# Performance work log

Measured on AMD Instinct MI355X. Metric: run time of the kernel, lower is better.

The kernel has to match this reference:

```python
import jax, jax.numpy as jnp
import numpy as np

SIDE = 64; EMB = 16; CH = 64; K = 64; V = 64; L = 8
N = SIDE * SIDE

def _pos_table(side, d):
    pe = np.array([[p / np.power(10000, 2 * (j // 2) / d) for j in range(d)]
                   if p != 0 else np.zeros(d) for p in range(side)])
    pe[1:, 0::2] = np.sin(pe[1:, 0::2])
    pe[1:, 1::2] = np.cos(pe[1:, 1::2])
    return pe.astype(np.float32)  # [side, d]

def _pos_emb():
    # Replicates torch .view(1, emb, side, 1): plain reshape of [side, emb] -> [emb, side]
    t = _pos_table(SIDE, EMB).reshape(EMB, SIDE)
    xe = np.broadcast_to(t[:, :, None], (EMB, SIDE, SIDE))
    ye = np.broadcast_to(t[:, None, :], (EMB, SIDE, SIDE))
    return jnp.asarray(np.concatenate([xe, ye], 0).reshape(1, 2 * EMB, N))

def _conv_mask():
    # CausalConv mask, see_center=False, 5x5: zero center pixel onward in center row, and all rows below
    m = np.ones((CH, 3, 5, 5), np.float32)
    m[:, :, 2, 2:] = 0.0
    m[:, :, 3:, :] = 0.0
    return jnp.asarray(m)

def _lrelu(x):
    return jnp.where(x >= 0, x, 0.01 * x)  # LeakyReLU(0.01)

def _bn(x, g, b, eps=1e-5):
    # training-mode batch norm (biased variance), channel axis = 1
    axes = (0,) + tuple(range(2, x.ndim))
    m = jnp.mean(x, axes, keepdims=True)
    var = jnp.mean((x - m) ** 2, axes, keepdims=True)
    sh = (1, -1) + (1,) * (x.ndim - 2)
    return g.reshape(sh) * (x - m) / jnp.sqrt(var + eps) + b.reshape(sh)

def _cv1(w, b, x):
    # 1x1 Conv1d: [O,I] x [B,I,N] -> [B,O,N]
    return jnp.einsum('oi,bin->bon', w, x) + b[:, None]

def reference(x, conv_w, conv_b, bn0_g, bn0_b, q_w, q_b, fk_w, fk_b, ck_w, ck_b,
              fv_w, fv_b, cv_w, cv_b, bn_g, bn_b, out_w, out_b):
    B = x.shape[0]
    pos = jnp.broadcast_to(_pos_emb(), (B, 2 * EMB, N))
    mask = jnp.tril(jnp.ones((N, N), jnp.float32))

    # masked causal conv input layer + BN + LeakyReLU
    w = conv_w * _conv_mask()
    h = jax.lax.conv_general_dilated(x, w, (1, 1), [(2, 2), (2, 2)],
                                     dimension_numbers=('NCHW', 'OIHW', 'NCHW'))
    h = h + conv_b[None, :, None, None]
    h = _lrelu(_bn(h, bn0_g, bn0_b)).reshape(B, CH, N)

    k0 = jnp.zeros((B, K, N), x.dtype)
    v0 = jnp.zeros((B, V, N), x.dtype)
    inv_sqrt_k = 1.0 / jnp.sqrt(jnp.float32(K))

    def layer(carry, p):
        h, k, v = carry
        qw, qb, fkw, fkb, ckw, ckb, fvw, fvb, cvw, cvb, g, bb = p
        x0 = jnp.concatenate([h, pos], 1)            # [B, CH+32, N]
        x0k = jnp.concatenate([x0, k], 1)            # [B, 160, N]
        x0v = jnp.concatenate([x0, v], 1)
        fk = jax.nn.sigmoid(_cv1(fkw, fkb, x0k))
        ck = _lrelu(_cv1(ckw, ckb, x0k))
        k_new = fk * k + ck                          # highway-gated persistent K
        fv = jax.nn.sigmoid(_cv1(fvw, fvb, x0v))
        cv_ = _lrelu(_cv1(cvw, cvb, x0v))
        v_new = fv * v + cv_
        q = _lrelu(_cv1(qw, qb, x0))                 # [B, K, N]
        attn = jnp.einsum('bkn,bkm->bnm', q, k) * inv_sqrt_k  # uses OLD k
        attn = attn * mask + (1.0 - mask) * (-10000.0)
        attn = jax.nn.softmax(attn, axis=-1) * mask
        out1 = jnp.einsum('bnm,bvm->bvn', attn, v)   # uses OLD v; [B, V, N]
        # original code computes fc(out1) but discards it (out2 overwritten)
        h2 = _lrelu(_bn(out1, g, bb))
        return (h2, k_new, v_new), None

    params = (q_w, q_b, fk_w, fk_b, ck_w, ck_b, fv_w, fv_b, cv_w, cv_b, bn_g, bn_b)
    (h, k, v), _ = jax.lax.scan(layer, (h, k0, v0), params)

    out = jnp.einsum('oi,bin->bon', out_w, h) + out_b[None, :, None]
    return out.reshape(B, out_w.shape[0], SIDE, SIDE)

def setup_inputs() -> dict:
    key = jax.random.key(0)
    ks = jax.random.split(key, 12)
    s = 0.05
    return {
        'x': jax.random.normal(ks[0], (2, 3, 64, 64), jnp.float32),
        'conv_w': jax.random.normal(ks[1], (CH, 3, 5, 5), jnp.float32) * s,
        'conv_b': jnp.zeros((CH,), jnp.float32),
        'bn0_g': jnp.ones((CH,), jnp.float32),
        'bn0_b': jnp.zeros((CH,), jnp.float32),
        'q_w': jax.random.normal(ks[2], (L, K, CH + 2 * EMB), jnp.float32) * s,
        'q_b': jnp.zeros((L, K), jnp.float32),
        'fk_w': jax.random.normal(ks[3], (L, K, CH + K + 2 * EMB), jnp.float32) * s,
        'fk_b': jnp.zeros((L, K), jnp.float32),
        'ck_w': jax.random.normal(ks[4], (L, K, CH + K + 2 * EMB), jnp.float32) * s,
        'ck_b': jnp.zeros((L, K), jnp.float32),
        'fv_w': jax.random.normal(ks[5], (L, V, CH + V + 2 * EMB), jnp.float32) * s,
        'fv_b': jnp.zeros((L, V), jnp.float32),
        'cv_w': jax.random.normal(ks[6], (L, V, CH + V + 2 * EMB), jnp.float32) * s,
        'cv_b': jnp.zeros((L, V), jnp.float32),
        'bn_g': jnp.ones((L, CH), jnp.float32),
        'bn_b': jnp.zeros((L, CH), jnp.float32),
        'out_w': jax.random.normal(ks[7], (100, V), jnp.float32) * s,
        'out_b': jnp.zeros((100,), jnp.float32),
    }
```

## Files before the change

kernel.cpp:

```cpp
#include <hip/hip_runtime.h>

#define NPIX 4096
#define CHN  64

typedef __attribute__((ext_vector_type(8))) short short8;
typedef __attribute__((ext_vector_type(8))) unsigned short ushort8;
typedef __attribute__((ext_vector_type(4))) unsigned short ushort4v;
typedef __attribute__((ext_vector_type(4))) float f32x4;
typedef __attribute__((ext_vector_type(16))) float f32x16;
typedef __attribute__((ext_vector_type(4))) unsigned int uint4v;

__device__ __forceinline__ float lrelu_(float x){ return x >= 0.f ? x : 0.01f*x; }

__device__ __forceinline__ unsigned short f2bf(float x){
  union { float f; unsigned u; } v; v.f = x;
  unsigned r = v.u + 0x7FFF + ((v.u >> 16) & 1);
  return (unsigned short)(r >> 16);
}
__device__ __forceinline__ float bf2f(unsigned short h){
  union { unsigned u; float f; } v; v.u = ((unsigned)h) << 16;
  return v.f;
}
__device__ __forceinline__ float asf_(unsigned u){
  union { unsigned u; float f; } v; v.u = u; return v.f;
}

__global__ void pos_kernel(float* __restrict__ pos){
  int idx = blockIdx.x*256 + threadIdx.x;
  int c = idx >> 12;
  int n = idx & (NPIX-1);
  int bcoord = (c < 16) ? (n >> 6) : (n & 63);
  int a = (c < 16) ? c : (c - 16);
  int flat = a*64 + bcoord;
  int p = flat >> 4;
  int j = flat & 15;
  float val = 0.f;
  if (p != 0){
    float ex = (float)(j & ~1) * (1.f/16.f);
    float w = powf(10000.f, -ex);
    float ang = (float)p * w;
    val = (j & 1) ? cosf(ang) : sinf(ang);
  }
  pos[idx] = val;
}

__global__ void wtr_kernel(const float* __restrict__ qw, const float* __restrict__ fkw,
                           const float* __restrict__ ckw, const float* __restrict__ fvw,
                           const float* __restrict__ cvw, const float* __restrict__ convw,
                           float* __restrict__ wt){
  int idx = blockIdx.x*256 + threadIdx.x;
  if (idx >= 381632) return;
  if (idx < 49152){
    int l = idx / 6144, r = idx % 6144, i = r >> 6, o = r & 63;
    wt[idx] = qw[(l*64 + o)*96 + i];
  } else if (idx < 376832){
    int e = idx - 49152;
    int mat = e / 81920, r = e % 81920;
    int l = r / 10240, rr = r % 10240, i = rr >> 6, o = rr & 63;
    const float* src = (mat==0) ? fkw : (mat==1) ? ckw : (mat==2) ? fvw : cvw;
    wt[idx] = src[(l*64 + o)*160 + i];
  } else {
    int e = idx - 376832;
    int o = e & 63, tap = e >> 6;
    int ci = tap / 25, r = tap % 25;
    wt[idx] = convw[(o*3 + ci)*25 + r];
  }
}

__global__ __launch_bounds__(256) void conv_in_kernel(const float* __restrict__ x,
                                                      const float* __restrict__ cwt,
                                                      const float* __restrict__ cb,
                                                      float* __restrict__ out){
  int t = threadIdx.x;
  int o = t & 63;
  int sub = t >> 6;
  int bid = blockIdx.x;
  int b = bid >> 10;
  int n = ((bid & 1023) << 2) + sub;
  int y = n >> 6, xx = n & 63;
  float acc = cb[o];
  #pragma unroll
  for (int ci=0; ci<3; ++ci){
    const float* xp = x + ((b*3+ci)<<12);
    #pragma unroll
    for (int ky=0; ky<3; ++ky){
      int yy = y + ky - 2;
      if (yy < 0) continue;
      int nk = (ky==2) ? 2 : 5;
      #pragma unroll
      for (int kx=0; kx<5; ++kx){
        if (kx >= nk) break;
        int xc = xx + kx - 2;
        if (xc < 0 || xc > 63) continue;
        acc += xp[(yy<<6) + xc] * cwt[(ci*25 + ky*5 + kx)*64 + o];
      }
    }
  }
  out[(b*CHN+o)*NPIX + n] = acc;
}

__global__ __launch_bounds__(1024) void bn_stats_kernel(const float* __restrict__ xin,
                                                        float* __restrict__ stats){
  int c = blockIdx.x;
  int t = threadIdx.x;
  float s = 0.f, ss = 0.f;
  #pragma unroll
  for (int it=0; it<8; ++it){
    int idx = t + it*1024;
    float v = xin[(((idx>>12))*CHN + c)*NPIX + (idx & (NPIX-1))];
    s += v; ss += v*v;
  }
  #pragma unroll
  for (int o=1; o<64; o<<=1){ s += __shfl_xor(s,o); ss += __shfl_xor(ss,o); }
  __shared__ float ps[16], pq[16];
  if ((t & 63) == 0){ ps[t>>6] = s; pq[t>>6] = ss; }
  __syncthreads();
  if (t == 0){
    float S=0.f, Q=0.f;
    #pragma unroll
    for (int i=0;i<16;++i){ S += ps[i]; Q += pq[i]; }
    float mu = S*(1.f/8192.f);
    float var = Q*(1.f/8192.f) - mu*mu;
    var = fmaxf(var, 0.f);
    stats[c*2]   = mu;
    stats[c*2+1] = rsqrtf(var + 1e-5f);
  }
}

__global__ void bn_apply_kernel(const float* __restrict__ xin, const float* __restrict__ stats,
                                const float* __restrict__ g, const float* __restrict__ bb,
                                float* __restrict__ hout){
  int idx = blockIdx.x*256 + threadIdx.x;
  int e = idx << 2;
  int c = (e >> 12) & 63;
  float mu = stats[c*2], rstd = stats[c*2+1];
  float gain = g[c]*rstd;
  float beta = bb[c] - gain*mu;
  float4 v = *(const float4*)(xin + e);
  float4 r;
  r.x = lrelu_(gain*v.x + beta);
  r.y = lrelu_(gain*v.y + beta);
  r.z = lrelu_(gain*v.z + beta);
  r.w = lrelu_(gain*v.w + beta);
  *(float4*)(hout + e) = r;
}

__global__ __launch_bounds__(256) void bn_apply2_kernel(float* __restrict__ hbuf,
                                                        const float* __restrict__ psum,
                                                        const float* __restrict__ psq,
                                                        const float* __restrict__ g,
                                                        const float* __restrict__ bb){
  int bid = blockIdx.x;
  int ebase = bid << 10;
  int c = (ebase >> 12) & 63;
  int t = threadIdx.x;
  float s = psum[c*256 + t];
  float q = psq[c*256 + t];
  #pragma unroll
  for (int o=1; o<64; o<<=1){ s += __shfl_xor(s,o); q += __shfl_xor(q,o); }
  __shared__ float as[4], aq[4];
  if ((t & 63) == 0){ as[t>>6] = s; aq[t>>6] = q; }
  __syncthreads();
  float S = as[0]+as[1]+as[2]+as[3];
  float Q = aq[0]+aq[1]+aq[2]+aq[3];
  float mu = S*(1.f/8192.f);
  float var = fmaxf(Q*(1.f/8192.f) - mu*mu, 0.f);
  float rstd = rsqrtf(var + 1e-5f);
  float gain = g[c]*rstd;
  float beta = bb[c] - gain*mu;
  float4 v = *(const float4*)(hbuf + ebase + t*4);
  float4 r;
  r.x = lrelu_(gain*v.x + beta);
  r.y = lrelu_(gain*v.y + beta);
  r.z = lrelu_(gain*v.z + beta);
  r.w = lrelu_(gain*v.w + beta);
  *(float4*)(hbuf + ebase + t*4) = r;
}

__global__ __launch_bounds__(256) void cv1_kernel(
    const float* __restrict__ hbuf, const float* __restrict__ pos,
    const float* __restrict__ kold, const float* __restrict__ vold,
    const float* __restrict__ qwt,
    const float* __restrict__ fkwt, const float* __restrict__ ckwt,
    const float* __restrict__ fvwt, const float* __restrict__ cvwt,
    const float* __restrict__ qbi,  const float* __restrict__ fkb,
    const float* __restrict__ ckb,  const float* __restrict__ fvb,
    const float* __restrict__ cvb,
    unsigned short* __restrict__ qh, unsigned short* __restrict__ ql,
    float* __restrict__ knew, unsigned short* __restrict__ khn, unsigned short* __restrict__ kln,
    float* __restrict__ vnew, unsigned short* __restrict__ vhTn, unsigned short* __restrict__ vlTn)
{
  int t = threadIdx.x;
  int o  = t & 63;
  int wv = t >> 6;
  int b    = blockIdx.x >> 8;
  int tile = blockIdx.x & 255;
  int n0 = tile*16 + wv*4;

  const float* hb = hbuf + b*CHN*NPIX + n0;
  const float* kb = kold + b*CHN*NPIX + n0;
  const float* vb = vold + b*CHN*NPIX + n0;
  const float* pb = pos + n0;

  auto load4 = [&](const float* p, float* dst){
    float4 a = *(const float4*)p;
    dst[0]=a.x; dst[1]=a.y; dst[2]=a.z; dst[3]=a.w;
  };

  float x[4];
  long obase = (long)(b*CHN+o)*NPIX + n0;
  size_t nbase = ((size_t)b*NPIX + n0)*64 + o;

  {
    float aq[4];
    float bias = qbi[o];
    #pragma unroll
    for (int j=0;j<4;++j) aq[j]=bias;
    #pragma unroll 4
    for (int i=0;i<64;++i){
      load4(hb + i*NPIX, x);
      float w = qwt[i*64 + o];
      #pragma unroll
      for (int j=0;j<4;++j) aq[j] += w*x[j];
    }
    #pragma unroll 4
    for (int i=0;i<32;++i){
      load4(pb + i*NPIX, x);
      float w = qwt[(64+i)*64 + o];
      #pragma unroll
      for (int j=0;j<4;++j) aq[j] += w*x[j];
    }
    #pragma unroll
    for (int j=0;j<4;++j){
      float v = lrelu_(aq[j]) * 0.125f;
      unsigned short hb16 = f2bf(v);
      qh[nbase + (size_t)j*64] = hb16;
      ql[nbase + (size_t)j*64] = f2bf(v - bf2f(hb16));
    }
  }

  {
    float af[4], ac[4];
    float bf = fkb[o], bc = ckb[o];
    #pragma unroll
    for (int j=0;j<4;++j){ af[j]=bf; ac[j]=bc; }
    #pragma unroll 4
    for (int i=0;i<64;++i){
      load4(hb + i*NPIX, x);
      float wf = fkwt[i*64+o], wc = ckwt[i*64+o];
      #pragma unroll
      for (int j=0;j<4;++j){ af[j] += wf*x[j]; ac[j] += wc*x[j]; }
    }
    #pragma unroll 4
    for (int i=0;i<32;++i){
      load4(pb + i*NPIX, x);
      float wf = fkwt[(64+i)*64+o], wc = ckwt[(64+i)*64+o];
      #pragma unroll
      for (int j=0;j<4;++j){ af[j] += wf*x[j]; ac[j] += wc*x[j]; }
    }
    #pragma unroll 4
    for (int i=0;i<64;++i){
      load4(kb + i*NPIX, x);
      float wf = fkwt[(96+i)*64+o], wc = ckwt[(96+i)*64+o];
      #pragma unroll
      for (int j=0;j<4;++j){ af[j] += wf*x[j]; ac[j] += wc*x[j]; }
    }
    float kv[4];
    load4(kb + o*NPIX, kv);
    #pragma unroll
    for (int j=0;j<4;++j){
      float fk = 1.f/(1.f+__expf(-af[j]));
      float kn = fk*kv[j] + lrelu_(ac[j]);
      knew[obase+j] = kn;
      unsigned short hb16 = f2bf(kn);
      khn[nbase + (size_t)j*64] = hb16;
      kln[nbase + (size_t)j*64] = f2bf(kn - bf2f(hb16));
    }
  }

  {
    float af[4], ac[4];
    float bf = fvb[o], bc = cvb[o];
    #pragma unroll
    for (int j=0;j<4;++j){ af[j]=bf; ac[j]=bc; }
    #pragma unroll 4
    for (int i=0;i<64;++i){
      load4(hb + i*NPIX, x);
      float wf = fvwt[i*64+o], wc = cvwt[i*64+o];
      #pragma unroll
      for (int j=0;j<4;++j){ af[j] += wf*x[j]; ac[j] += wc*x[j]; }
    }
    #pragma unroll 4
    for (int i=0;i<32;++i){
      load4(pb + i*NPIX, x);
      float wf = fvwt[(64+i)*64+o], wc = cvwt[(64+i)*64+o];
      #pragma unroll
      for (int j=0;j<4;++j){ af[j] += wf*x[j]; ac[j] += wc*x[j]; }
    }
    #pragma unroll 4
    for (int i=0;i<64;++i){
      load4(vb + i*NPIX, x);
      float wf = fvwt[(96+i)*64+o], wc = cvwt[(96+i)*64+o];
      #pragma unroll
      for (int j=0;j<4;++j){ af[j] += wf*x[j]; ac[j] += wc*x[j]; }
    }
    float vv[4];
    load4(vb + o*NPIX, vv);
    ushort4v vph, vpl;
    #pragma unroll
    for (int j=0;j<4;++j){
      float fv = 1.f/(1.f+__expf(-af[j]));
      float vn = fv*vv[j] + lrelu_(ac[j]);
      vnew[obase+j] = vn;
      unsigned short hb16 = f2bf(vn);
      vph[j] = hb16;
      vpl[j] = f2bf(vn - bf2f(hb16));
    }
    *(ushort4v*)(vhTn + ((size_t)(b*CHN+o))*NPIX + n0) = vph;
    *(ushort4v*)(vlTn + ((size_t)(b*CHN+o))*NPIX + n0) = vpl;
  }
}

__device__ __forceinline__ void pack_sf(const f32x16& sfv, unsigned (&ph)[4][2],
                                        unsigned (&pl)[4][2]){
  #pragma unroll
  for (int a=0; a<4; ++a){
    unsigned h0, h1;
    asm("v_cvt_pk_bf16_f32 %0, %1, %2" : "=v"(h0) : "v"(sfv[4*a]),   "v"(sfv[4*a+1]));
    asm("v_cvt_pk_bf16_f32 %0, %1, %2" : "=v"(h1) : "v"(sfv[4*a+2]), "v"(sfv[4*a+3]));
    float r0 = sfv[4*a]   - asf_(h0 << 16);
    float r1 = sfv[4*a+1] - asf_(h0 & 0xffff0000u);
    float r2 = sfv[4*a+2] - asf_(h1 << 16);
    float r3 = sfv[4*a+3] - asf_(h1 & 0xffff0000u);
    unsigned l0, l1;
    asm("v_cvt_pk_bf16_f32 %0, %1, %2" : "=v"(l0) : "v"(r0), "v"(r1));
    asm("v_cvt_pk_bf16_f32 %0, %1, %2" : "=v"(l1) : "v"(r2), "v"(r3));
    ph[a][0]=h0; ph[a][1]=h1; pl[a][0]=l0; pl[a][1]=l1;
  }
}

__global__ __launch_bounds__(128) void attn_mfma(
    const unsigned short* __restrict__ qhg, const unsigned short* __restrict__ qlg,
    const unsigned short* __restrict__ khg, const unsigned short* __restrict__ klg,
    const unsigned short* __restrict__ vhg, const unsigned short* __restrict__ vlg,
    float* __restrict__ part)
{
  int bid = 575 - (int)blockIdx.x;
  int b = 0, id = bid;
  if (id >= 288){ b = 1; id -= 288; }
  int pidx = bid;
  int rem = id, k = 0;
  while (rem >= 8*(k+1)){ rem -= 8*(k+1); ++k; }
  int rt    = 8*k + rem/(k+1);
  int chunk = rem - (rem/(k+1))*(k+1);

  int C0  = chunk << 9;
  int end = min(C0 + 512, rt*64 + 64);
  int nt  = (end - C0 + 63) >> 6;

  int t = threadIdx.x;
  int w = t >> 6;
  int l = t & 63;
  int q = l & 31;
  int hi = l >> 5;
  int qbase = rt*64 + w*32;
  int n_g = qbase + q;
  int nmax_w = qbase + 31;

  __shared__ __align__(16) char KH[8192], KL[8192];
  __shared__ __align__(16) char VH[8192], VL[8192];

  const unsigned short* qhp = qhg + (size_t)b*NPIX*64;
  const unsigned short* qlp = qlg + (size_t)b*NPIX*64;
  const unsigned short* khp = khg + (size_t)b*NPIX*64;
  const unsigned short* klp = klg + (size_t)b*NPIX*64;
  const unsigned short* vhp = vhg + (size_t)b*CHN*NPIX;
  const unsigned short* vlp = vlg + (size_t)b*CHN*NPIX;

  short8 qhf[4], qlf[4];
  #pragma unroll
  for (int kc=0; kc<4; ++kc){
    qhf[kc] = *(const short8*)(qhp + (size_t)n_g*64 + kc*16 + hi*8);
    qlf[kc] = *(const short8*)(qlp + (size_t)n_g*64 + kc*16 + hi*8);
  }

  int srow[4], scc8[4], soff[4];
  #pragma unroll
  for (int p=0; p<4; ++p){
    int slot = t + (p<<7);
    int row = slot >> 3, cc = slot & 7;
    srow[p] = row; scc8[p] = cc*8;
    soff[p] = row*128 + ((cc ^ (row & 7)) << 4);
  }
  ushort8 rkh[4], rkl[4], rvh[4], rvl[4];
  auto issue = [&](int m0){
    #pragma unroll
    for (int p=0; p<4; ++p){
      rkh[p] = *(const ushort8*)(khp + (size_t)(m0+srow[p])*64 + scc8[p]);
      rkl[p] = *(const ushort8*)(klp + (size_t)(m0+srow[p])*64 + scc8[p]);
      rvh[p] = *(const ushort8*)(vhp + (size_t)srow[p]*NPIX + m0 + scc8[p]);
      rvl[p] = *(const ushort8*)(vlp + (size_t)srow[p]*NPIX + m0 + scc8[p]);
    }
  };

  f32x16 oacc0, oacc1;
  #pragma unroll
  for (int i=0; i<16; ++i){ oacc0[i]=0.f; oacc1[i]=0.f; }
  float m_run = -1e30f, l_run = 0.f;

  issue(C0);
  for (int ti=0; ti<nt; ++ti){
    int m0 = C0 + (ti<<6);
    __syncthreads();
    #pragma unroll
    for (int p=0; p<4; ++p){
      *(ushort8*)(KH + soff[p]) = rkh[p];
      *(ushort8*)(KL + soff[p]) = rkl[p];
      *(ushort8*)(VH + soff[p]) = rvh[p];
      *(ushort8*)(VL + soff[p]) = rvl[p];
    }
    __syncthreads();
    if (ti+1 < nt) issue(m0 + 64);

    if (m0 <= nmax_w){
      f32x16 sf0, sf1;
      #pragma unroll
      for (int i=0; i<16; ++i){ sf0[i]=0.f; sf1[i]=0.f; }
      #pragma unroll
      for (int kc=0; kc<4; ++kc){
        int off0 = q*128 + (((2*kc + hi) ^ (q & 7)) << 4);
        short8 ah0 = *(const short8*)(KH + off0);
        short8 al0 = *(const short8*)(KL + off0);
        short8 ah1 = *(const short8*)(KH + off0 + 4096);
        short8 al1 = *(const short8*)(KL + off0 + 4096);
        sf0 = __builtin_amdgcn_mfma_f32_32x32x16_bf16(ah0, qhf[kc], sf0, 0,0,0);
        sf1 = __builtin_amdgcn_mfma_f32_32x32x16_bf16(ah1, qhf[kc], sf1, 0,0,0);
        sf0 = __builtin_amdgcn_mfma_f32_32x32x16_bf16(al0, qhf[kc], sf0, 0,0,0);
        sf1 = __builtin_amdgcn_mfma_f32_32x32x16_bf16(al1, qhf[kc], sf1, 0,0,0);
        sf0 = __builtin_amdgcn_mfma_f32_32x32x16_bf16(ah0, qlf[kc], sf0, 0,0,0);
        sf1 = __builtin_amdgcn_mfma_f32_32x32x16_bf16(ah1, qlf[kc], sf1, 0,0,0);
      }
      float mx = -1e30f;
      #pragma unroll
      for (int r=0; r<16; ++r){
        int mg0 = m0 + (r&3) + 8*(r>>2) + 4*hi;
        float s0 = (mg0 <= n_g) ? sf0[r] : -1e30f;
        float s1 = (mg0 + 32 <= n_g) ? sf1[r] : -1e30f;
        sf0[r] = s0; sf1[r] = s1;
        mx = fmaxf(mx, fmaxf(s0, s1));
      }
      mx = fmaxf(mx, __shfl_xor(mx, 32));
      float m_new = fmaxf(m_run, mx);
      float alpha = __expf(m_run - m_new);
      float ps = 0.f;
      #pragma unroll
      for (int r=0; r<16; ++r){
        float e0 = __expf(sf0[r] - m_new);
        float e1 = __expf(sf1[r] - m_new);
        sf0[r] = e0; sf1[r] = e1;
        ps += e0 + e1;
      }
      ps += __shfl_xor(ps, 32);
      l_run = l_run*alpha + ps;
      m_run = m_new;

      unsigned ph0[4][2], pl0[4][2], ph1[4][2], pl1[4][2];
      pack_sf(sf0, ph0, pl0);
      pack_sf(sf1, ph1, pl1);

      #pragma unroll
      for (int i=0; i<16; ++i){ oacc0[i] *= alpha; oacc1[i] *= alpha; }

#define PV_KC(KC, PH, PL) { \
      const int kk = (KC)&1; \
      unsigned oh0 = hi ? PH[2*kk+1][0] : PH[2*kk][0]; \
      unsigned oh1 = hi ? PH[2*kk+1][1] : PH[2*kk][1]; \
      unsigned sh0 = hi ? PH[2*kk][0]   : PH[2*kk+1][0]; \
      unsigned sh1 = hi ? PH[2*kk][1]   : PH[2*kk+1][1]; \
      unsigned rh0 = __shfl_xor(sh0, 32); \
      unsigned rh1 = __shfl_xor(sh1, 32); \
      unsigned ol0 = hi ? PL[2*kk+1][0] : PL[2*kk][0]; \
      unsigned ol1 = hi ? PL[2*kk+1][1] : PL[2*kk][1]; \
      unsigned sl0 = hi ? PL[2*kk][0]   : PL[2*kk+1][0]; \
      unsigned sl1 = hi ? PL[2*kk][1]   : PL[2*kk+1][1]; \
      unsigned rl0 = __shfl_xor(sl0, 32); \
      unsigned rl1 = __shfl_xor(sl1, 32); \
      union { uint4v u; short8 s; } fh, fl; \
      fh.u[0] = hi ? rh0 : oh0; fh.u[1] = hi ? rh1 : oh1; \
      fh.u[2] = hi ? oh0 : rh0; fh.u[3] = hi ? oh1 : rh1; \
      fl.u[0] = hi ? rl0 : ol0; fl.u[1] = hi ? rl1 : ol1; \
      fl.u[2] = hi ? ol0 : rl0; fl.u[3] = hi ? ol1 : rl1; \
      int poff = q*128 + (((2*(KC) + hi) ^ (q & 7)) << 4); \
      short8 xvh0 = *(const short8*)(VH + poff); \
      short8 xvl0 = *(const short8*)(VL + poff); \
      short8 xvh1 = *(const short8*)(VH + poff + 4096); \
      short8 xvl1 = *(const short8*)(VL + poff + 4096); \
      oacc0 = __builtin_amdgcn_mfma_f32_32x32x16_bf16(xvh0, fh.s, oacc0, 0,0,0); \
      oacc1 = __builtin_amdgcn_mfma_f32_32x32x16_bf16(xvh1, fh.s, oacc1, 0,0,0); \
      oacc0 = __builtin_amdgcn_mfma_f32_32x32x16_bf16(xvl0, fh.s, oacc0, 0,0,0); \
      oacc1 = __builtin_amdgcn_mfma_f32_32x32x16_bf16(xvl1, fh.s, oacc1, 0,0,0); \
      oacc0 = __builtin_amdgcn_mfma_f32_32x32x16_bf16(xvh0, fl.s, oacc0, 0,0,0); \
      oacc1 = __builtin_amdgcn_mfma_f32_32x32x16_bf16(xvh1, fl.s, oacc1, 0,0,0); \
    }
      PV_KC(0, ph0, pl0)
      PV_KC(1, ph0, pl0)
      PV_KC(2, ph1, pl1)
      PV_KC(3, ph1, pl1)
#undef PV_KC
    }
  }

  float* pacc = part + (size_t)pidx * 4224;
  #pragma unroll
  for (int vf=0; vf<2; ++vf){
    #pragma unroll
    for (int qd=0; qd<4; ++qd){
      int vd = 32*vf + 8*qd + 4*hi;
      f32x4 vv;
      vv.x = vf ? oacc1[4*qd]   : oacc0[4*qd];
      vv.y = vf ? oacc1[4*qd+1] : oacc0[4*qd+1];
      vv.z = vf ? oacc1[4*qd+2] : oacc0[4*qd+2];
      vv.w = vf ? oacc1[4*qd+3] : oacc0[4*qd+3];
      *(f32x4*)(pacc + (size_t)(w*32 + q)*64 + vd) = vv;
    }
  }
  if (l < 32){
    pacc[4096 + (w*32 + l)*2]     = m_run;
    pacc[4096 + (w*32 + l)*2 + 1] = l_run;
  }
}

__global__ __launch_bounds__(256) void attn_combine(const float* __restrict__ part,
                                                    float* __restrict__ out1,
                                                    float* __restrict__ psum,
                                                    float* __restrict__ psq){
  int bid = blockIdx.x;
  int b = bid >> 7, rt = bid & 127;
  int rt64 = rt >> 1;
  int k2 = rt64 >> 3;
  int nch = k2 + 1;
  int base = b*288 + 4*k2*(k2+1) + (rt64 - 8*k2)*nch;

  int t = threadIdx.x;
  int nl = t & 31, vq = t >> 5;
  int row64 = (rt & 1)*32 + nl;

  float M = -1e30f;
  #pragma unroll
  for (int c=0; c<8; ++c)
    if (c < nch) M = fmaxf(M, part[(size_t)(base+c)*4224 + 4096 + row64*2]);

  float L = 0.f;
  float val[8];
  #pragma unroll
  for (int jj=0; jj<8; ++jj) val[jj] = 0.f;
  #pragma unroll
  for (int c=0; c<8; ++c){
    if (c < nch){
      const float* pa = part + (size_t)(base+c)*4224;
      float wgt = __expf(pa[4096 + row64*2] - M);
      L += pa[4096 + row64*2 + 1] * wgt;
      #pragma unroll
      for (int jj=0; jj<8; ++jj) val[jj] += wgt * pa[row64*64 + vq*8 + jj];
    }
  }
  float invL = 1.f / L;
  float s[8], q[8];
  #pragma unroll
  for (int jj=0; jj<8; ++jj){
    float v = val[jj]*invL;
    out1[((size_t)b*CHN + vq*8 + jj)*NPIX + rt*32 + nl] = v;
    s[jj] = v; q[jj] = v*v;
  }
  #pragma unroll
  for (int o2=1; o2<32; o2<<=1){
    #pragma unroll
    for (int jj=0; jj<8; ++jj){
      s[jj] += __shfl_xor(s[jj], o2);
      q[jj] += __shfl_xor(q[jj], o2);
    }
  }
  if (nl == 0){
    #pragma unroll
    for (int jj=0; jj<8; ++jj){
      int c = vq*8 + jj;
      psum[c*256 + bid] = s[jj];
      psq [c*256 + bid] = q[jj];
    }
  }
}

__global__ __launch_bounds__(256) void final_kernel(const float* __restrict__ h,
                                                    const float* __restrict__ ow,
                                                    const float* __restrict__ ob,
                                                    float* __restrict__ out){
  int idx = blockIdx.x*256 + threadIdx.x;
  int b  = idx / 409600;
  int r  = idx - b*409600;
  int oc = r >> 12;
  int n  = r & (NPIX-1);
  const float* hp = h + (size_t)b*CHN*NPIX + n;
  const float* wp = ow + oc*64;
  float acc = ob[oc];
  #pragma unroll
  for (int v=0; v<64; ++v) acc += wp[v]*hp[(size_t)v*NPIX];
  out[idx] = acc;
}

extern "C" void kernel_launch(void* const* d_in, const int* in_sizes, int n_in,
                              void* d_out, int out_size, void* d_ws, size_t ws_size,
                              hipStream_t stream){
  const float* x     = (const float*)d_in[0];
  const float* convw = (const float*)d_in[1];
  const float* convb = (const float*)d_in[2];
  const float* bn0g  = (const float*)d_in[3];
  const float* bn0b  = (const float*)d_in[4];
  const float* qw    = (const float*)d_in[5];
  const float* qbias = (const float*)d_in[6];
  const float* fkw   = (const float*)d_in[7];
  const float* fkb   = (const float*)d_in[8];
  const float* ckw   = (const float*)d_in[9];
  const float* ckb   = (const float*)d_in[10];
  const float* fvw   = (const float*)d_in[11];
  const float* fvb   = (const float*)d_in[12];
  const float* cvw   = (const float*)d_in[13];
  const float* cvb   = (const float*)d_in[14];
  const float* bng   = (const float*)d_in[15];
  const float* bnb   = (const float*)d_in[16];
  const float* ow    = (const float*)d_in[17];
  const float* ob    = (const float*)d_in[18];

  const size_t TEN = (size_t)2*CHN*NPIX;
  const size_t BFU = TEN/2;
  float* ws   = (float*)d_ws;
  float* pos  = ws;
  float* h    = pos + 32*NPIX;
  float* k0   = h  + TEN;
  float* k1   = k0 + TEN;
  float* v0   = k1 + TEN;
  float* v1   = v0 + TEN;
  float* stats = v1 + TEN;
  float* psum = stats + 128;
  float* psq  = psum + 64*256;
  float* wt   = psq + 64*256;
  float* bfb  = wt + 381632;
  unsigned short* qh  = (unsigned short*)(bfb);
  unsigned short* ql  = (unsigned short*)(bfb + BFU);
  unsigned short* kh0 = (unsigned short*)(bfb + 2*BFU);
  unsigned short* kh1 = (unsigned short*)(bfb + 3*BFU);
  unsigned short* kl0 = (unsigned short*)(bfb + 4*BFU);
  unsigned short* kl1 = (unsigned short*)(bfb + 5*BFU);
  unsigned short* vh0 = (unsigned short*)(bfb + 6*BFU);
  unsigned short* vh1 = (unsigned short*)(bfb + 7*BFU);
  unsigned short* vl0 = (unsigned short*)(bfb + 8*BFU);
  unsigned short* vl1 = (unsigned short*)(bfb + 9*BFU);
  float* part = bfb + 10*BFU;

  hipMemsetAsync(k0, 0, TEN*sizeof(float), stream);
  hipMemsetAsync(v0, 0, TEN*sizeof(float), stream);
  hipMemsetAsync(kh0, 0, TEN*2, stream);
  hipMemsetAsync(kl0, 0, TEN*2, stream);
  hipMemsetAsync(vh0, 0, TEN*2, stream);
  hipMemsetAsync(vl0, 0, TEN*2, stream);

  pos_kernel<<<512,256,0,stream>>>(pos);
  wtr_kernel<<<1491,256,0,stream>>>(qw, fkw, ckw, fvw, cvw, convw, wt);
  conv_in_kernel<<<2048,256,0,stream>>>(x, wt + 376832, convb, h);
  bn_stats_kernel<<<64,1024,0,stream>>>(h, stats);
  bn_apply_kernel<<<512,256,0,stream>>>(h, stats, bn0g, bn0b, h);

  float* kfp[2] = {k0,k1};
  float* vfp[2] = {v0,v1};
  unsigned short* khb[2] = {kh0,kh1};
  unsigned short* klb[2] = {kl0,kl1};
  unsigned short* vhb[2] = {vh0,vh1};
  unsigned short* vlb[2] = {vl0,vl1};
  for (int l=0; l<8; ++l){
    float* kold = kfp[l&1]; float* knew = kfp[(l+1)&1];
    float* vold = vfp[l&1]; float* vnew = vfp[(l+1)&1];
    cv1_kernel<<<512,256,0,stream>>>(h, pos, kold, vold,
        wt + l*6144,
        wt + 49152 + l*10240,
        wt + 49152 + 81920 + l*10240,
        wt + 49152 + 2*81920 + l*10240,
        wt + 49152 + 3*81920 + l*10240,
        qbias + l*64, fkb + l*64, ckb + l*64, fvb + l*64, cvb + l*64,
        qh, ql,
        knew, khb[(l+1)&1], klb[(l+1)&1],
        vnew, vhb[(l+1)&1], vlb[(l+1)&1]);
    attn_mfma<<<576,128,0,stream>>>(qh, ql, khb[l&1], klb[l&1], vhb[l&1], vlb[l&1], part);
    attn_combine<<<256,256,0,stream>>>(part, h, psum, psq);
    bn_apply2_kernel<<<512,256,0,stream>>>(h, psum, psq, bng + l*64, bnb + l*64);
  }
  final_kernel<<<3200,256,0,stream>>>(h, ow, ob, (float*)d_out);
}
```

Baseline: 857.7 us.

## Halve attention KV chunk size, use exp2 softmax, drop fp32 V buffer

Attention key/value chunks shrink from 512 to 256 columns, so the grid grows from 576 to 1088 blocks to give more parallelism and better load balance across CUs, and the combine kernel merges up to 16 partials. The log2(e) factor is folded into the query scale so the softmax can use exp2f instead of __expf. The fp32 V state buffer is removed and the split bf16 hi/lo V copies are read back in cv1, which cuts memory traffic and one memset. In exchange, the combine step has more partial-buffer traffic and the V state is reconstructed from the bf16 pair.

Measured after the change: 898.5 us. +4.8%, slower.

```diff
diff --git a/kernel.cpp b/kernel.cpp
--- a/kernel.cpp
+++ b/kernel.cpp
@@ -179,7 +179,8 @@
 
 __global__ __launch_bounds__(256) void cv1_kernel(
     const float* __restrict__ hbuf, const float* __restrict__ pos,
-    const float* __restrict__ kold, const float* __restrict__ vold,
+    const float* __restrict__ kold,
+    const unsigned short* __restrict__ vhTo, const unsigned short* __restrict__ vlTo,
     const float* __restrict__ qwt,
     const float* __restrict__ fkwt, const float* __restrict__ ckwt,
     const float* __restrict__ fvwt, const float* __restrict__ cvwt,
@@ -188,7 +189,7 @@
     const float* __restrict__ cvb,
     unsigned short* __restrict__ qh, unsigned short* __restrict__ ql,
     float* __restrict__ knew, unsigned short* __restrict__ khn, unsigned short* __restrict__ kln,
-    float* __restrict__ vnew, unsigned short* __restrict__ vhTn, unsigned short* __restrict__ vlTn)
+    unsigned short* __restrict__ vhTn, unsigned short* __restrict__ vlTn)
 {
   int t = threadIdx.x;
   int o  = t & 63;
@@ -199,7 +200,8 @@
 
   const float* hb = hbuf + b*CHN*NPIX + n0;
   const float* kb = kold + b*CHN*NPIX + n0;
-  const float* vb = vold + b*CHN*NPIX + n0;
+  const unsigned short* vhb_ = vhTo + (size_t)(b*CHN)*NPIX + n0;
+  const unsigned short* vlb_ = vlTo + (size_t)(b*CHN)*NPIX + n0;
   const float* pb = pos + n0;
 
   auto load4 = [&](const float* p, float* dst){
@@ -232,7 +234,7 @@
     }
     #pragma unroll
     for (int j=0;j<4;++j){
-      float v = lrelu_(aq[j]) * 0.125f;
+      float v = lrelu_(aq[j]) * (0.125f * 1.4426950408889634f);
       unsigned short hb16 = f2bf(v);
       qh[nbase + (size_t)j*64] = hb16;
       ql[nbase + (size_t)j*64] = f2bf(v - bf2f(hb16));
@@ -299,19 +301,23 @@
     }
     #pragma unroll 4
     for (int i=0;i<64;++i){
-      load4(vb + i*NPIX, x);
+      ushort4v xh = *(const ushort4v*)(vhb_ + (size_t)i*NPIX);
+      ushort4v xl = *(const ushort4v*)(vlb_ + (size_t)i*NPIX);
       float wf = fvwt[(96+i)*64+o], wc = cvwt[(96+i)*64+o];
       #pragma unroll
-      for (int j=0;j<4;++j){ af[j] += wf*x[j]; ac[j] += wc*x[j]; }
-    }
-    float vv[4];
-    load4(vb + o*NPIX, vv);
+      for (int j=0;j<4;++j){
+        float xv = bf2f(xh[j]) + bf2f(xl[j]);
+        af[j] += wf*xv; ac[j] += wc*xv;
+      }
+    }
+    ushort4v vvh = *(const ushort4v*)(vhb_ + (size_t)o*NPIX);
+    ushort4v vvl = *(const ushort4v*)(vlb_ + (size_t)o*NPIX);
     ushort4v vph, vpl;
     #pragma unroll
     for (int j=0;j<4;++j){
       float fv = 1.f/(1.f+__expf(-af[j]));
-      float vn = fv*vv[j] + lrelu_(ac[j]);
-      vnew[obase+j] = vn;
+      float vold_ = bf2f(vvh[j]) + bf2f(vvl[j]);
+      float vn = fv*vold_ + lrelu_(ac[j]);
       unsigned short hb16 = f2bf(vn);
       vph[j] = hb16;
       vpl[j] = f2bf(vn - bf2f(hb16));
@@ -345,17 +351,17 @@
     const unsigned short* __restrict__ vhg, const unsigned short* __restrict__ vlg,
     float* __restrict__ part)
 {
-  int bid = 575 - (int)blockIdx.x;
+  int bid = 1087 - (int)blockIdx.x;
   int b = 0, id = bid;
-  if (id >= 288){ b = 1; id -= 288; }
+  if (id >= 544){ b = 1; id -= 544; }
   int pidx = bid;
   int rem = id, k = 0;
-  while (rem >= 8*(k+1)){ rem -= 8*(k+1); ++k; }
-  int rt    = 8*k + rem/(k+1);
+  while (rem >= 4*(k+1)){ rem -= 4*(k+1); ++k; }
+  int rt    = 4*k + rem/(k+1);
   int chunk = rem - (rem/(k+1))*(k+1);
 
-  int C0  = chunk << 9;
-  int end = min(C0 + 512, rt*64 + 64);
+  int C0  = chunk << 8;
+  int end = min(C0 + 256, rt*64 + 64);
   int nt  = (end - C0 + 63) >> 6;
 
   int t = threadIdx.x;
@@ -451,12 +457,12 @@
       }
       mx = fmaxf(mx, __shfl_xor(mx, 32));
       float m_new = fmaxf(m_run, mx);
-      float alpha = __expf(m_run - m_new);
+      float alpha = exp2f(m_run - m_new);
       float ps = 0.f;
       #pragma unroll
       for (int r=0; r<16; ++r){
-        float e0 = __expf(sf0[r] - m_new);
-        float e1 = __expf(sf1[r] - m_new);
+        float e0 = exp2f(sf0[r] - m_new);
+        float e1 = exp2f(sf1[r] - m_new);
         sf0[r] = e0; sf1[r] = e1;
         ps += e0 + e1;
       }
@@ -537,9 +543,9 @@
   int bid = blockIdx.x;
   int b = bid >> 7, rt = bid & 127;
   int rt64 = rt >> 1;
-  int k2 = rt64 >> 3;
-  int nch = k2 + 1;
-  int base = b*288 + 4*k2*(k2+1) + (rt64 - 8*k2)*nch;
+  int g2 = rt64 >> 2;
+  int nch = g2 + 1;
+  int base = b*544 + 2*g2*(g2+1) + (rt64 & 3)*(g2+1);
 
   int t = threadIdx.x;
   int nl = t & 31, vq = t >> 5;
@@ -547,7 +553,7 @@
 
   float M = -1e30f;
   #pragma unroll
-  for (int c=0; c<8; ++c)
+  for (int c=0; c<16; ++c)
     if (c < nch) M = fmaxf(M, part[(size_t)(base+c)*4224 + 4096 + row64*2]);
 
   float L = 0.f;
@@ -555,10 +561,10 @@
   #pragma unroll
   for (int jj=0; jj<8; ++jj) val[jj] = 0.f;
   #pragma unroll
-  for (int c=0; c<8; ++c){
+  for (int c=0; c<16; ++c){
     if (c < nch){
       const float* pa = part + (size_t)(base+c)*4224;
-      float wgt = __expf(pa[4096 + row64*2] - M);
+      float wgt = exp2f(pa[4096 + row64*2] - M);
       L += pa[4096 + row64*2 + 1] * wgt;
       #pragma unroll
       for (int jj=0; jj<8; ++jj) val[jj] += wgt * pa[row64*64 + vq*8 + jj];
@@ -637,9 +643,7 @@
   float* h    = pos + 32*NPIX;
   float* k0   = h  + TEN;
   float* k1   = k0 + TEN;
-  float* v0   = k1 + TEN;
-  float* v1   = v0 + TEN;
-  float* stats = v1 + TEN;
+  float* stats = k1 + TEN;
   float* psum = stats + 128;
   float* psq  = psum + 64*256;
   float* wt   = psq + 64*256;
@@ -657,7 +661,6 @@
   float* part = bfb + 10*BFU;
 
   hipMemsetAsync(k0, 0, TEN*sizeof(float), stream);
-  hipMemsetAsync(v0, 0, TEN*sizeof(float), stream);
   hipMemsetAsync(kh0, 0, TEN*2, stream);
   hipMemsetAsync(kl0, 0, TEN*2, stream);
   hipMemsetAsync(vh0, 0, TEN*2, stream);
@@ -670,15 +673,13 @@
   bn_apply_kernel<<<512,256,0,stream>>>(h, stats, bn0g, bn0b, h);
 
   float* kfp[2] = {k0,k1};
-  float* vfp[2] = {v0,v1};
   unsigned short* khb[2] = {kh0,kh1};
   unsigned short* klb[2] = {kl0,kl1};
   unsigned short* vhb[2] = {vh0,vh1};
   unsigned short* vlb[2] = {vl0,vl1};
   for (int l=0; l<8; ++l){
     float* kold = kfp[l&1]; float* knew = kfp[(l+1)&1];
-    float* vold = vfp[l&1]; float* vnew = vfp[(l+1)&1];
-    cv1_kernel<<<512,256,0,stream>>>(h, pos, kold, vold,
+    cv1_kernel<<<512,256,0,stream>>>(h, pos, kold, vhb[l&1], vlb[l&1],
         wt + l*6144,
         wt + 49152 + l*10240,
         wt + 49152 + 81920 + l*10240,
@@ -687,8 +688,8 @@
         qbias + l*64, fkb + l*64, ckb + l*64, fvb + l*64, cvb + l*64,
         qh, ql,
         knew, khb[(l+1)&1], klb[(l+1)&1],
-        vnew, vhb[(l+1)&1], vlb[(l+1)&1]);
-    attn_mfma<<<576,128,0,stream>>>(qh, ql, khb[l&1], klb[l&1], vhb[l&1], vlb[l&1], part);
+        vhb[(l+1)&1], vlb[(l+1)&1]);
+    attn_mfma<<<1088,128,0,stream>>>(qh, ql, khb[l&1], klb[l&1], vhb[l&1], vlb[l&1], part);
     attn_combine<<<256,256,0,stream>>>(part, h, psum, psq);
     bn_apply2_kernel<<<512,256,0,stream>>>(h, psum, psq, bng + l*64, bnb + l*64);
   }
```

## Split projection kernel into q/k/v sections and halve attention chunk size

Applied to the files above, without the earlier changes.

The 1x1-projection kernel now launches three times as many blocks, each computing only one of the q, k or v sections instead of all three in sequence. The causal attention splits key ranges into 256-wide chunks instead of 512, roughly doubling the number of blocks, and the combine kernel's indexing is updated to merge up to 16 partials. The softmax scale now folds in log2(e) so exp2f replaces __expf. The aim is more blocks to fill the GPU's compute units and shorter per-block latency, at the cost of re-reading h and pos per section and writing and combining more partial results.

After: 854.9 us. About the same (-0.3%).

```diff
diff --git a/kernel.cpp b/kernel.cpp
--- a/kernel.cpp
+++ b/kernel.cpp
@@ -193,13 +193,13 @@
   int t = threadIdx.x;
   int o  = t & 63;
   int wv = t >> 6;
-  int b    = blockIdx.x >> 8;
-  int tile = blockIdx.x & 255;
+  int sec  = blockIdx.x >> 9;
+  int bid  = blockIdx.x & 511;
+  int b    = bid >> 8;
+  int tile = bid & 255;
   int n0 = tile*16 + wv*4;
 
   const float* hb = hbuf + b*CHN*NPIX + n0;
-  const float* kb = kold + b*CHN*NPIX + n0;
-  const float* vb = vold + b*CHN*NPIX + n0;
   const float* pb = pos + n0;
 
   auto load4 = [&](const float* p, float* dst){
@@ -211,7 +211,7 @@
   long obase = (long)(b*CHN+o)*NPIX + n0;
   size_t nbase = ((size_t)b*NPIX + n0)*64 + o;
 
-  {
+  if (sec == 0){
     float aq[4];
     float bias = qbi[o];
     #pragma unroll
@@ -230,16 +230,16 @@
       #pragma unroll
       for (int j=0;j<4;++j) aq[j] += w*x[j];
     }
+    const float QS = 0.125f * 1.4426950408889634f;
     #pragma unroll
     for (int j=0;j<4;++j){
-      float v = lrelu_(aq[j]) * 0.125f;
+      float v = lrelu_(aq[j]) * QS;
       unsigned short hb16 = f2bf(v);
       qh[nbase + (size_t)j*64] = hb16;
       ql[nbase + (size_t)j*64] = f2bf(v - bf2f(hb16));
     }
-  }
-
-  {
+  } else if (sec == 1){
+    const float* kb = kold + b*CHN*NPIX + n0;
     float af[4], ac[4];
     float bf = fkb[o], bc = ckb[o];
     #pragma unroll
@@ -276,9 +276,8 @@
       khn[nbase + (size_t)j*64] = hb16;
       kln[nbase + (size_t)j*64] = f2bf(kn - bf2f(hb16));
     }
-  }
-
-  {
+  } else {
+    const float* vb = vold + b*CHN*NPIX + n0;
     float af[4], ac[4];
     float bf = fvb[o], bc = cvb[o];
     #pragma unroll
@@ -345,17 +344,17 @@
     const unsigned short* __restrict__ vhg, const unsigned short* __restrict__ vlg,
     float* __restrict__ part)
 {
-  int bid = 575 - (int)blockIdx.x;
+  int bid = 1087 - (int)blockIdx.x;
   int b = 0, id = bid;
-  if (id >= 288){ b = 1; id -= 288; }
+  if (id >= 544){ b = 1; id -= 544; }
   int pidx = bid;
   int rem = id, k = 0;
-  while (rem >= 8*(k+1)){ rem -= 8*(k+1); ++k; }
-  int rt    = 8*k + rem/(k+1);
+  while (rem >= 4*(k+1)){ rem -= 4*(k+1); ++k; }
+  int rt    = 4*k + rem/(k+1);
   int chunk = rem - (rem/(k+1))*(k+1);
 
-  int C0  = chunk << 9;
-  int end = min(C0 + 512, rt*64 + 64);
+  int C0  = chunk << 8;
+  int end = min(C0 + 256, rt*64 + 64);
   int nt  = (end - C0 + 63) >> 6;
 
   int t = threadIdx.x;
@@ -451,12 +450,12 @@
       }
       mx = fmaxf(mx, __shfl_xor(mx, 32));
       float m_new = fmaxf(m_run, mx);
-      float alpha = __expf(m_run - m_new);
+      float alpha = exp2f(m_run - m_new);
       float ps = 0.f;
       #pragma unroll
       for (int r=0; r<16; ++r){
-        float e0 = __expf(sf0[r] - m_new);
-        float e1 = __expf(sf1[r] - m_new);
+        float e0 = exp2f(sf0[r] - m_new);
+        float e1 = exp2f(sf1[r] - m_new);
         sf0[r] = e0; sf1[r] = e1;
         ps += e0 + e1;
       }
@@ -537,9 +536,9 @@
   int bid = blockIdx.x;
   int b = bid >> 7, rt = bid & 127;
   int rt64 = rt >> 1;
-  int k2 = rt64 >> 3;
-  int nch = k2 + 1;
-  int base = b*288 + 4*k2*(k2+1) + (rt64 - 8*k2)*nch;
+  int g2 = rt64 >> 2;
+  int nch = g2 + 1;
+  int base = b*544 + 2*g2*(g2+1) + (rt64 & 3)*(g2+1);
 
   int t = threadIdx.x;
   int nl = t & 31, vq = t >> 5;
@@ -547,7 +546,7 @@
 
   float M = -1e30f;
   #pragma unroll
-  for (int c=0; c<8; ++c)
+  for (int c=0; c<16; ++c)
     if (c < nch) M = fmaxf(M, part[(size_t)(base+c)*4224 + 4096 + row64*2]);
 
   float L = 0.f;
@@ -555,10 +554,10 @@
   #pragma unroll
   for (int jj=0; jj<8; ++jj) val[jj] = 0.f;
   #pragma unroll
-  for (int c=0; c<8; ++c){
+  for (int c=0; c<16; ++c){
     if (c < nch){
       const float* pa = part + (size_t)(base+c)*4224;
-      float wgt = __expf(pa[4096 + row64*2] - M);
+      float wgt = exp2f(pa[4096 + row64*2] - M);
       L += pa[4096 + row64*2 + 1] * wgt;
       #pragma unroll
       for (int jj=0; jj<8; ++jj) val[jj] += wgt * pa[row64*64 + vq*8 + jj];
@@ -678,7 +677,7 @@
   for (int l=0; l<8; ++l){
     float* kold = kfp[l&1]; float* knew = kfp[(l+1)&1];
     float* vold = vfp[l&1]; float* vnew = vfp[(l+1)&1];
-    cv1_kernel<<<512,256,0,stream>>>(h, pos, kold, vold,
+    cv1_kernel<<<1536,256,0,stream>>>(h, pos, kold, vold,
         wt + l*6144,
         wt + 49152 + l*10240,
         wt + 49152 + 81920 + l*10240,
@@ -688,7 +687,7 @@
         qh, ql,
         knew, khb[(l+1)&1], klb[(l+1)&1],
         vnew, vhb[(l+1)&1], vlb[(l+1)&1]);
-    attn_mfma<<<576,128,0,stream>>>(qh, ql, khb[l&1], klb[l&1], vhb[l&1], vlb[l&1], part);
+    attn_mfma<<<1088,128,0,stream>>>(qh, ql, khb[l&1], klb[l&1], vhb[l&1], vlb[l&1], part);
     attn_combine<<<256,256,0,stream>>>(part, h, psum, psq);
     bn_apply2_kernel<<<512,256,0,stream>>>(h, psum, psq, bng + l*64, bnb + l*64);
   }
```
